# Performance work log

Measured on AMD Instinct MI355X. Metric: run time of the kernel, lower is better.

Reference implementation:

```python
import math
import jax, jax.numpy as jnp
import numpy as np

C, NH, NL, NP, NLAYERS, FFN = 256, 8, 3, 4, 6, 1024
DH = C // NH
SHAPES = ((64, 64), (32, 32), (16, 16))  # (H,W) for res3, res4, res5
SIZES = [h * w for h, w in SHAPES]
STARTS = np.cumsum([0] + SIZES[:-1]).tolist()
EPS = 1e-5


def _sin_pe(H, W):
    d = C // 4
    y = jnp.arange(H, dtype=jnp.float32)[:, None]
    x = jnp.arange(W, dtype=jnp.float32)[None, :]
    div = jnp.exp(jnp.arange(d, dtype=jnp.float32) * (-math.log(10000.0) / d))[:, None, None]
    pe = jnp.concatenate([
        jnp.broadcast_to(jnp.sin(y * div), (d, H, W)),
        jnp.broadcast_to(jnp.cos(y * div), (d, H, W)),
        jnp.broadcast_to(jnp.sin(x * div), (d, H, W)),
        jnp.broadcast_to(jnp.cos(x * div), (d, H, W)),
    ], axis=0)  # (C,H,W)
    return pe.reshape(C, H * W).T  # (HW, C)


def _ref_points():
    pts = []
    for H, W in SHAPES:
        y = jnp.linspace(0.5 / H, 1.0 - 0.5 / H, H)
        x = jnp.linspace(0.5 / W, 1.0 - 0.5 / W, W)
        ry, rx = jnp.meshgrid(y, x, indexing='ij')
        pts.append(jnp.stack([rx.ravel(), ry.ravel()], -1))
    return jnp.concatenate(pts, 0)[None, :, None, :]  # (1,N,1,2), same per level


def _layernorm(x, g, b):
    mu = x.mean(-1, keepdims=True)
    v = ((x - mu) ** 2).mean(-1, keepdims=True)
    return (x - mu) * jax.lax.rsqrt(v + EPS) * g + b


def _bilinear(v, loc, H, W):
    # v: (B,HW,NH,DH); loc: (B,N,NH,NP,2) in [0,1]; grid_sample align_corners=False, zero pad
    B, N = loc.shape[0], loc.shape[1]
    x = loc[..., 0] * W - 0.5
    y = loc[..., 1] * H - 0.5
    x0 = jnp.floor(x); y0 = jnp.floor(y)
    wx = x - x0; wy = y - y0
    x0i = x0.astype(jnp.int32); y0i = y0.astype(jnp.int32)
    v_t = jnp.transpose(v, (0, 2, 1, 3))  # (B,NH,HW,DH)

    def corner(xi, yi, w):
        valid = (xi >= 0) & (xi < W) & (yi >= 0) & (yi < H)
        idx = jnp.clip(yi, 0, H - 1) * W + jnp.clip(xi, 0, W - 1)  # (B,N,NH,NP)
        idx = jnp.transpose(idx, (0, 2, 1, 3)).reshape(B, NH, N * NP)
        g = jnp.take_along_axis(v_t, idx[..., None], axis=2)  # (B,NH,N*NP,DH)
        g = g.reshape(B, NH, N, NP, DH).transpose(0, 2, 1, 3, 4)
        return g * (w * valid)[..., None]

    return (corner(x0i, y0i, (1 - wx) * (1 - wy))
            + corner(x0i + 1, y0i, wx * (1 - wy))
            + corner(x0i, y0i + 1, (1 - wx) * wy)
            + corner(x0i + 1, y0i + 1, wx * wy))


def _forward(res2, res3, res4, res5, level_embed, off_W, off_b, aw_W, aw_b, val_W, val_b,
             out_W, out_b, ln1_g, ln1_b, fc1_W, fc1_b, fc2_W, fc2_b, ln2_g, ln2_b,
             lat_W, lat_b, sm_W, sm_b, gn_g, gn_b):
    feats = [res3, res4, res5]
    B = res3.shape[0]
    flat = jnp.concatenate(
        [f.reshape(B, C, -1).transpose(0, 2, 1) + level_embed[i] for i, f in enumerate(feats)], 1)
    pe = jnp.concatenate([_sin_pe(H, W) for H, W in SHAPES], 0)[None]  # (1,N,C)
    ref = _ref_points()  # (1,N,1,2)
    normalizer = jnp.array([[W, H] for H, W in SHAPES], jnp.float32)  # (NL,2) as (W,H)
    N = flat.shape[1]

    x = flat
    for l in range(NLAYERS):
        q = x + pe
        value = (x @ val_W[l].T + val_b[l]).reshape(B, N, NH, DH)
        off = (q @ off_W[l].T + off_b[l]).reshape(B, N, NH, NL, NP, 2)
        aw = jax.nn.softmax((q @ aw_W[l].T + aw_b[l]).reshape(B, N, NH, NL * NP), -1)
        aw = aw.reshape(B, N, NH, NL, NP)
        loc = ref[:, :, None, :, None, :] + off / normalizer[None, None, None, :, None, :]
        attn = jnp.zeros((B, N, NH, DH), x.dtype)
        for li, (H, W) in enumerate(SHAPES):
            v_l = value[:, STARTS[li]:STARTS[li] + SIZES[li]]
            samp = _bilinear(v_l, loc[:, :, :, li], H, W)  # (B,N,NH,NP,DH)
            attn = attn + jnp.einsum('bnhpd,bnhp->bnhd', samp, aw[:, :, :, li])
        attn = attn.reshape(B, N, C) @ out_W[l].T + out_b[l]
        x = _layernorm(x + attn, ln1_g[l], ln1_b[l])
        h = jax.nn.relu(x @ fc1_W[l].T + fc1_b[l]) @ fc2_W[l].T + fc2_b[l]
        x = _layernorm(x + h, ln2_g[l], ln2_b[l])

    outs = []
    for li, (H, W) in enumerate(SHAPES):
        tok = x[:, STARTS[li]:STARTS[li] + SIZES[li]]
        outs.append(tok.transpose(0, 2, 1).reshape(B, C, H, W))
    o3, o4, o5 = outs

    r2_lat = jnp.einsum('bchw,oc->bohw', res2, lat_W) + lat_b[None, :, None, None]
    Hr, Wr = res2.shape[2], res2.shape[3]
    r3_up = jax.image.resize(o3, (B, C, Hr, Wr), method='bilinear')
    s = jax.lax.conv_general_dilated(r2_lat + r3_up, sm_W, (1, 1), ((1, 1), (1, 1)),
                                     dimension_numbers=('NCHW', 'OIHW', 'NCHW'))
    s = s + sm_b[None, :, None, None]
    # GroupNorm(32, C)
    g = s.reshape(B, 32, C // 32, Hr, Wr)
    mu = g.mean((2, 3, 4), keepdims=True)
    var = jnp.var(g, axis=(2, 3, 4), keepdims=True)
    g = (g - mu) * jax.lax.rsqrt(var + EPS)
    s = g.reshape(B, C, Hr, Wr) * gn_g[None, :, None, None] + gn_b[None, :, None, None]
    s = jax.nn.gelu(s, approximate=False)
    return s, o3, o4, o5


def setup_inputs() -> dict:
    key = jax.random.key(0)
    ks = jax.random.split(key, 16)
    def rn(k, shape, s=0.02):
        return jax.random.normal(k, shape, jnp.float32) * s
    B = 2
    L = NLAYERS
    return {
        'res2': jax.random.normal(ks[0], (B, C, 128, 128), jnp.float32),
        'res3': jax.random.normal(ks[1], (B, C, 64, 64), jnp.float32),
        'res4': jax.random.normal(ks[2], (B, C, 32, 32), jnp.float32),
        'res5': jax.random.normal(ks[3], (B, C, 16, 16), jnp.float32),
        'level_embed': rn(ks[4], (NL, C)),
        'off_W': rn(ks[5], (L, NH * NL * NP * 2, C)), 'off_b': jnp.zeros((L, NH * NL * NP * 2)),
        'aw_W': rn(ks[6], (L, NH * NL * NP, C)), 'aw_b': jnp.zeros((L, NH * NL * NP)),
        'val_W': rn(ks[7], (L, C, C)), 'val_b': jnp.zeros((L, C)),
        'out_W': rn(ks[8], (L, C, C)), 'out_b': jnp.zeros((L, C)),
        'ln1_g': jnp.ones((L, C)), 'ln1_b': jnp.zeros((L, C)),
        'fc1_W': rn(ks[9], (L, FFN, C)), 'fc1_b': jnp.zeros((L, FFN)),
        'fc2_W': rn(ks[10], (L, C, FFN)), 'fc2_b': jnp.zeros((L, C)),
        'ln2_g': jnp.ones((L, C)), 'ln2_b': jnp.zeros((L, C)),
        'lat_W': rn(ks[11], (C, C)), 'lat_b': jnp.zeros((C,)),
        'sm_W': rn(ks[12], (C, C, 3, 3)), 'sm_b': jnp.zeros((C,)),
        'gn_g': jnp.ones((C,)), 'gn_b': jnp.zeros((C,)),
    }


def reference(res2, res3, res4, res5, level_embed, off_W, off_b, aw_W, aw_b, val_W, val_b,
              out_W, out_b, ln1_g, ln1_b, fc1_W, fc1_b, fc2_W, fc2_b, ln2_g, ln2_b,
              lat_W, lat_b, sm_W, sm_b, gn_g, gn_b):
    return _forward(res2, res3, res4, res5, level_embed, off_W, off_b, aw_W, aw_b,
                    val_W, val_b, out_W, out_b, ln1_g, ln1_b, fc1_W, fc1_b, fc2_W, fc2_b,
                    ln2_g, ln2_b, lat_W, lat_b, sm_W, sm_b, gn_g, gn_b)
```

## Files before the change

### kernel.cpp

```cpp
#include <hip/hip_runtime.h>

namespace {
constexpr int Bn   = 2;
constexpr int Cc   = 256;
constexpr int Ntok = 5376;
constexpr int Ffn  = 1024;
constexpr int HW2  = 128 * 128;
constexpr float EPSf = 1e-5f;
constexpr int WL   = 729088;
}

typedef __attribute__((ext_vector_type(8))) short bf16x8;
typedef __attribute__((ext_vector_type(4))) float f32x4;

__device__ inline unsigned short f2bf(float x) {
  unsigned u = __float_as_uint(x);
  return (unsigned short)((u + 0x7fffu + ((u >> 16) & 1u)) >> 16);
}
__device__ inline float bf2f(unsigned short b) {
  return __uint_as_float((unsigned)b << 16);
}

__device__ inline void store_chunk_f32(unsigned short* lds, int row, int g,
                                       const float* v8) {
  int sg = g ^ (row & 7);
  unsigned short tmp[8];
#pragma unroll
  for (int j = 0; j < 8; j++) tmp[j] = f2bf(v8[j]);
  *reinterpret_cast<uint4*>(&lds[row * 64 + sg * 8]) =
      *reinterpret_cast<const uint4*>(tmp);
}
__device__ inline void store_chunk_bf(unsigned short* lds, int row, int g,
                                      uint4 v) {
  int sg = g ^ (row & 7);
  *reinterpret_cast<uint4*>(&lds[row * 64 + sg * 8]) = v;
}

__global__ __launch_bounds__(256) void setup_all(
    const float* __restrict__ r3, const float* __restrict__ r4,
    const float* __restrict__ r5, const float* __restrict__ lemb,
    float* __restrict__ x, unsigned short* __restrict__ xb,
    unsigned short* __restrict__ qb, unsigned short* __restrict__ peb,
    const float* __restrict__ valW, const float* __restrict__ offW,
    const float* __restrict__ awW, const float* __restrict__ outW,
    const float* __restrict__ fc1W, const float* __restrict__ fc2W,
    const float* __restrict__ latW, const float* __restrict__ smW,
    unsigned short* __restrict__ wbf, unsigned short* __restrict__ wlat,
    unsigned short* __restrict__ wt) {
  int bx = blockIdx.x;
  int tid = threadIdx.x;
  if (bx < 1024) {
    const int NPC = Ntok * Cc;
    for (int i = bx * 256 + tid; i < Bn * NPC; i += 1024 * 256) {
      int c = i & 255;
      int rest = i >> 8;
      int p = rest % Ntok;
      int b = rest / Ntok;
      int li = (p < 4096) ? 0 : ((p < 5120) ? 1 : 2);
      int start = (li == 0) ? 0 : ((li == 1) ? 4096 : 5120);
      int size = (li == 0) ? 4096 : ((li == 1) ? 1024 : 256);
      const float* f = (li == 0) ? r3 : ((li == 1) ? r4 : r5);
      int sp = p - start;
      int shift = 6 - li;
      int W = 64 >> li;
      int iy = sp >> shift;
      int ix = sp & (W - 1);
      int j = c & 63;
      int sel = c >> 6;
      float div = expf(-(float)j * (9.210340371976184f / 64.f));
      float coord = (sel < 2) ? (float)iy : (float)ix;
      float arg = coord * div;
      unsigned short pe16 = f2bf((sel & 1) ? cosf(arg) : sinf(arg));
      float v = f[((size_t)(b * Cc + c)) * size + sp] + lemb[li * Cc + c];
      x[i] = v;
      xb[i] = f2bf(v);
      qb[i] = f2bf(v + bf2f(pe16));
      peb[i - b * NPC] = pe16;
    }
    return;
  }
  int b2 = bx - 1024;
  if (b2 < 4272) {
    int i4 = b2 * 256 + tid;
    int l = i4 / 182272;
    int e = (i4 - l * 182272) * 4;
    const float* src;
    int off;
    if (e < 65536) { src = valW + (size_t)l * 65536; off = e; }
    else if (e < 139264) {
      int j = e - 65536;
      if (j < 49152) { src = offW + (size_t)l * 49152; off = j; }
      else { src = awW + (size_t)l * 24576; off = j - 49152; }
    } else if (e < 204800) { src = outW + (size_t)l * 65536; off = e - 139264; }
    else if (e < 466944) { src = fc1W + (size_t)l * 262144; off = e - 204800; }
    else { src = fc2W + (size_t)l * 262144; off = e - 466944; }
    float4 v = *reinterpret_cast<const float4*>(&src[off]);
    unsigned short t[4] = {f2bf(v.x), f2bf(v.y), f2bf(v.z), f2bf(v.w)};
    *reinterpret_cast<uint2*>(&wbf[(size_t)l * WL + e]) =
        *reinterpret_cast<const uint2*>(t);
  } else if (b2 < 4336) {
    int e = ((b2 - 4272) * 256 + tid) * 4;
    float4 v = *reinterpret_cast<const float4*>(&latW[e]);
    unsigned short t[4] = {f2bf(v.x), f2bf(v.y), f2bf(v.z), f2bf(v.w)};
    *reinterpret_cast<uint2*>(&wlat[e]) = *reinterpret_cast<const uint2*>(t);
  } else {
    int i = (b2 - 4336) * 256 + tid;
    int o = i / 2304;
    int r = i - o * 2304;
    int tap = r >> 8;
    int c = r & 255;
    wt[i] = f2bf(smW[((size_t)(o * 256 + c)) * 9 + tap]);
  }
}

template <int ACT, int OBF>
__global__ __launch_bounds__(256) void gemm_mfma_b(
    const unsigned short* __restrict__ A, const unsigned short* __restrict__ Wb,
    const float* __restrict__ bias, void* __restrict__ outp,
    int M, int N, int K, int nbx) {
  __shared__ unsigned short As[64 * 64];
  __shared__ unsigned short Ws[128 * 64];
  const int tid = threadIdx.x;
  const int nwg = gridDim.x;
  const int swz = (blockIdx.x & 7) * (nwg >> 3) + (blockIdx.x >> 3);
  const int m0 = (swz / nbx) * 64, n0 = (swz % nbx) * 128;
  const int wid = tid >> 6, lane = tid & 63;
  const int wm = wid >> 1, wn = wid & 1;
  const int lr = lane & 15, lh = lane >> 4;
  const int r8 = tid >> 3, g8 = tid & 7;
  f32x4 acc[2][4];
#pragma unroll
  for (int i = 0; i < 2; i++)
#pragma unroll
    for (int j = 0; j < 4; j++) acc[i][j] = f32x4{0.f, 0.f, 0.f, 0.f};

  uint4 ra[2], rw[4];
  const uint4 z4 = uint4{0, 0, 0, 0};
#pragma unroll
  for (int i = 0; i < 2; i++)
    ra[i] = *reinterpret_cast<const uint4*>(
        &A[(size_t)(m0 + r8 + i * 32) * K + g8 * 8]);
#pragma unroll
  for (int i = 0; i < 4; i++) {
    int n = n0 + r8 + i * 32;
    rw[i] = (n < N) ? *reinterpret_cast<const uint4*>(
                          &Wb[(size_t)n * K + g8 * 8])
                    : z4;
  }

  for (int k0 = 0; k0 < K; k0 += 64) {
    if (k0) __syncthreads();
#pragma unroll
    for (int i = 0; i < 2; i++) store_chunk_bf(As, r8 + i * 32, g8, ra[i]);
#pragma unroll
    for (int i = 0; i < 4; i++) store_chunk_bf(Ws, r8 + i * 32, g8, rw[i]);
    __syncthreads();
    int kn = k0 + 64;
    if (kn < K) {
#pragma unroll
      for (int i = 0; i < 2; i++)
        ra[i] = *reinterpret_cast<const uint4*>(
            &A[(size_t)(m0 + r8 + i * 32) * K + kn + g8 * 8]);
#pragma unroll
      for (int i = 0; i < 4; i++) {
        int n = n0 + r8 + i * 32;
        rw[i] = (n < N) ? *reinterpret_cast<const uint4*>(
                              &Wb[(size_t)n * K + kn + g8 * 8])
                        : z4;
      }
    }
    bf16x8 af[2][2], bfr[4][2];
#pragma unroll
    for (int mi = 0; mi < 2; mi++) {
      int r = wm * 32 + mi * 16 + lr;
#pragma unroll
      for (int s = 0; s < 2; s++) {
        int g = s * 4 + lh;
        af[mi][s] =
            *reinterpret_cast<const bf16x8*>(&As[r * 64 + (g ^ (r & 7)) * 8]);
      }
    }
#pragma unroll
    for (int nj = 0; nj < 4; nj++) {
      int r = wn * 64 + nj * 16 + lr;
#pragma unroll
      for (int s = 0; s < 2; s++) {
        int g = s * 4 + lh;
        bfr[nj][s] =
            *reinterpret_cast<const bf16x8*>(&Ws[r * 64 + (g ^ (r & 7)) * 8]);
      }
    }
#pragma unroll
    for (int mi = 0; mi < 2; mi++)
#pragma unroll
      for (int nj = 0; nj < 4; nj++) {
        acc[mi][nj] = __builtin_amdgcn_mfma_f32_16x16x32_bf16(
            af[mi][0], bfr[nj][0], acc[mi][nj], 0, 0, 0);
        acc[mi][nj] = __builtin_amdgcn_mfma_f32_16x16x32_bf16(
            af[mi][1], bfr[nj][1], acc[mi][nj], 0, 0, 0);
      }
  }
#pragma unroll
  for (int mi = 0; mi < 2; mi++) {
    int row = m0 + wm * 32 + mi * 16 + lh * 4;
#pragma unroll
    for (int nj = 0; nj < 4; nj++) {
      int col = n0 + wn * 64 + nj * 16 + lr;
      if (col >= N) continue;
      float b = bias[col];
#pragma unroll
      for (int r = 0; r < 4; r++) {
        float v = acc[mi][nj][r] + b;
        if (ACT) v = fmaxf(v, 0.f);
        if (OBF)
          ((unsigned short*)outp)[(size_t)(row + r) * N + col] = f2bf(v);
        else
          ((float*)outp)[(size_t)(row + r) * N + col] = v;
      }
    }
  }
}

template <int WRITEQ, int TOKOUT>
__global__ __launch_bounds__(256) void gemm_ln(
    const unsigned short* __restrict__ A, const unsigned short* __restrict__ Wb,
    const float* __restrict__ bias, const float* __restrict__ g,
    const float* __restrict__ bta, float* __restrict__ x,
    unsigned short* __restrict__ xb, const unsigned short* __restrict__ peb,
    unsigned short* __restrict__ qb, int K, float* __restrict__ o3,
    float* __restrict__ o4, float* __restrict__ o5) {
  __shared__ unsigned short As[16 * 64];
  __shared__ unsigned short Ws[256 * 64];
  __shared__ float pred[4][16];
  __shared__ float qred[4][16];
  const int tid = threadIdx.x;
  const int swz = (blockIdx.x & 7) * 84 + (blockIdx.x >> 3);
  const int m0 = swz * 16;
  const int wid = tid >> 6, lane = tid & 63;
  const int lr = lane & 15, lh = lane >> 4;
  const int r8 = tid >> 3, g8 = tid & 7;
  f32x4 acc[4];
#pragma unroll
  for (int i = 0; i < 4; i++) acc[i] = f32x4{0.f, 0.f, 0.f, 0.f};

  uint4 ra, rw[8];
  if (tid < 128)
    ra = *reinterpret_cast<const uint4*>(&A[(size_t)(m0 + r8) * K + g8 * 8]);
#pragma unroll
  for (int i = 0; i < 8; i++)
    rw[i] = *reinterpret_cast<const uint4*>(
        &Wb[(size_t)(r8 + i * 32) * K + g8 * 8]);

  for (int k0 = 0; k0 < K; k0 += 64) {
    if (k0) __syncthreads();
    if (tid < 128) store_chunk_bf(As, r8, g8, ra);
#pragma unroll
    for (int i = 0; i < 8; i++) store_chunk_bf(Ws, r8 + i * 32, g8, rw[i]);
    __syncthreads();
    int kn = k0 + 64;
    if (kn < K) {
      if (tid < 128)
        ra = *reinterpret_cast<const uint4*>(
            &A[(size_t)(m0 + r8) * K + kn + g8 * 8]);
#pragma unroll
      for (int i = 0; i < 8; i++)
        rw[i] = *reinterpret_cast<const uint4*>(
            &Wb[(size_t)(r8 + i * 32) * K + kn + g8 * 8]);
    }
    bf16x8 af[2];
    {
      int r = lr;
#pragma unroll
      for (int s = 0; s < 2; s++) {
        int gg2 = s * 4 + lh;
        af[s] =
            *reinterpret_cast<const bf16x8*>(&As[r * 64 + (gg2 ^ (r & 7)) * 8]);
      }
    }
#pragma unroll
    for (int nt = 0; nt < 4; nt++) {
      int r = wid * 64 + nt * 16 + lr;
      bf16x8 b0 =
          *reinterpret_cast<const bf16x8*>(&Ws[r * 64 + (lh ^ (r & 7)) * 8]);
      bf16x8 b1 = *reinterpret_cast<const bf16x8*>(
          &Ws[r * 64 + ((4 + lh) ^ (r & 7)) * 8]);
      acc[nt] =
          __builtin_amdgcn_mfma_f32_16x16x32_bf16(af[0], b0, acc[nt], 0, 0, 0);
      acc[nt] =
          __builtin_amdgcn_mfma_f32_16x16x32_bf16(af[1], b1, acc[nt], 0, 0, 0);
    }
  }

  const int rowl = lh * 4;
#pragma unroll
  for (int nt = 0; nt < 4; nt++) {
    int col = wid * 64 + nt * 16 + lr;
    float bs = bias[col];
#pragma unroll
    for (int r = 0; r < 4; r++)
      acc[nt][r] += bs + x[(size_t)(m0 + rowl + r) * 256 + col];
  }
  float sum[4];
#pragma unroll
  for (int r = 0; r < 4; r++) {
    float s = 0.f;
#pragma unroll
    for (int nt = 0; nt < 4; nt++) s += acc[nt][r];
#pragma unroll
    for (int o = 8; o > 0; o >>= 1) s += __shfl_xor(s, o);
    sum[r] = s;
  }
  if (lr == 0) {
#pragma unroll
    for (int r = 0; r < 4; r++) pred[wid][lh * 4 + r] = sum[r];
  }
  __syncthreads();
  float mu[4];
#pragma unroll
  for (int r = 0; r < 4; r++)
    mu[r] = (pred[0][lh * 4 + r] + pred[1][lh * 4 + r] + pred[2][lh * 4 + r] +
             pred[3][lh * 4 + r]) *
            (1.f / 256.f);
  float qs[4];
#pragma unroll
  for (int r = 0; r < 4; r++) {
    float q = 0.f;
#pragma unroll
    for (int nt = 0; nt < 4; nt++) {
      float d = acc[nt][r] - mu[r];
      q += d * d;
    }
#pragma unroll
    for (int o = 8; o > 0; o >>= 1) q += __shfl_xor(q, o);
    qs[r] = q;
  }
  if (lr == 0) {
#pragma unroll
    for (int r = 0; r < 4; r++) qred[wid][lh * 4 + r] = qs[r];
  }
  __syncthreads();
  float rstd[4];
#pragma unroll
  for (int r = 0; r < 4; r++)
    rstd[r] = rsqrtf((qred[0][lh * 4 + r] + qred[1][lh * 4 + r] +
                      qred[2][lh * 4 + r] + qred[3][lh * 4 + r]) *
                         (1.f / 256.f) +
                     EPSf);
  float oarr[4][4];
#pragma unroll
  for (int nt = 0; nt < 4; nt++) {
    int col = wid * 64 + nt * 16 + lr;
    float gw = g[col], bw = bta[col];
#pragma unroll
    for (int r = 0; r < 4; r++) {
      int row = m0 + rowl + r;
      size_t idx = (size_t)row * 256 + col;
      float o = (acc[nt][r] - mu[r]) * rstd[r] * gw + bw;
      x[idx] = o;
      xb[idx] = f2bf(o);
      if (WRITEQ) {
        size_t pc = idx - (row >= Ntok ? (size_t)Ntok * 256 : 0);
        qb[idx] = f2bf(o + bf2f(peb[pc]));
      }
      if (TOKOUT) oarr[nt][r] = o;
    }
  }
  if constexpr (TOKOUT) {
    __shared__ float tout[16][129];
    int bb = (m0 >= Ntok) ? 1 : 0;
    int n = m0 - bb * Ntok;
    float* outp;
    int osize, ostart;
    if (n < 4096) { outp = o3; osize = 4096; ostart = 0; }
    else if (n < 5120) { outp = o4; osize = 1024; ostart = 4096; }
    else { outp = o5; osize = 256; ostart = 5120; }
    int sp0 = n - ostart;
#pragma unroll
    for (int hh = 0; hh < 2; hh++) {
      __syncthreads();
      if ((wid >> 1) == hh) {
#pragma unroll
        for (int nt = 0; nt < 4; nt++) {
          int cl = (wid & 1) * 64 + nt * 16 + lr;
#pragma unroll
          for (int r = 0; r < 4; r++) tout[rowl + r][cl] = oarr[nt][r];
        }
      }
      __syncthreads();
      int cl = tid & 127, rh = tid >> 7;
      float* dst =
          outp + ((size_t)(bb * 256 + hh * 128 + cl)) * osize + sp0 + rh * 8;
#pragma unroll
      for (int i = 0; i < 8; i += 4) {
        float4 v4 = {tout[rh * 8 + i + 0][cl], tout[rh * 8 + i + 1][cl],
                     tout[rh * 8 + i + 2][cl], tout[rh * 8 + i + 3][cl]};
        *reinterpret_cast<float4*>(&dst[i]) = v4;
      }
    }
  }
}

__global__ __launch_bounds__(256) void gemm_head(
    const unsigned short* __restrict__ xb, const unsigned short* __restrict__ qb,
    const unsigned short* __restrict__ wv, const unsigned short* __restrict__ wo,
    const float* __restrict__ valB, const float* __restrict__ offB,
    const float* __restrict__ awB, unsigned short* __restrict__ valO,
    float* __restrict__ offO, float* __restrict__ awO) {
  __shared__ unsigned short As[32 * 64];
  __shared__ unsigned short Ws[128 * 64];
  const int tid = threadIdx.x;
  const int swz = (blockIdx.x & 7) * 210 + (blockIdx.x >> 3);
  const bool isval = swz < 672;
  const unsigned short* A;
  const unsigned short* W;
  int m0, n0, Nn;
  if (isval) {
    A = xb; W = wv; Nn = 256;
    m0 = (swz >> 1) * 32; n0 = (swz & 1) * 128;
  } else {
    int s = swz - 672;
    A = qb; W = wo; Nn = 288;
    m0 = (s / 3) * 32; n0 = (s % 3) * 128;
  }
  const int wid = tid >> 6, lane = tid & 63;
  const int wm = wid >> 1, wn = wid & 1;
  const int lr = lane & 15, lh = lane >> 4;
  const int r8 = tid >> 3, g8 = tid & 7;
  f32x4 acc[4];
#pragma unroll
  for (int j = 0; j < 4; j++) acc[j] = f32x4{0.f, 0.f, 0.f, 0.f};

  uint4 ra, rw[4];
  const uint4 z4 = uint4{0, 0, 0, 0};
  ra = *reinterpret_cast<const uint4*>(&A[(size_t)(m0 + r8) * 256 + g8 * 8]);
#pragma unroll
  for (int i = 0; i < 4; i++) {
    int n = n0 + r8 + i * 32;
    rw[i] = (n < Nn) ? *reinterpret_cast<const uint4*>(
                           &W[(size_t)n * 256 + g8 * 8])
                     : z4;
  }

  for (int k0 = 0; k0 < 256; k0 += 64) {
    if (k0) __syncthreads();
    store_chunk_bf(As, r8, g8, ra);
#pragma unroll
    for (int i = 0; i < 4; i++) store_chunk_bf(Ws, r8 + i * 32, g8, rw[i]);
    __syncthreads();
    int kn = k0 + 64;
    if (kn < 256) {
      ra = *reinterpret_cast<const uint4*>(
          &A[(size_t)(m0 + r8) * 256 + kn + g8 * 8]);
#pragma unroll
      for (int i = 0; i < 4; i++) {
        int n = n0 + r8 + i * 32;
        rw[i] = (n < Nn) ? *reinterpret_cast<const uint4*>(
                               &W[(size_t)n * 256 + kn + g8 * 8])
                         : z4;
      }
    }
    bf16x8 af[2];
    {
      int r = wm * 16 + lr;
#pragma unroll
      for (int s = 0; s < 2; s++) {
        int gg2 = s * 4 + lh;
        af[s] =
            *reinterpret_cast<const bf16x8*>(&As[r * 64 + (gg2 ^ (r & 7)) * 8]);
      }
    }
#pragma unroll
    for (int nj = 0; nj < 4; nj++) {
      int r = wn * 64 + nj * 16 + lr;
      bf16x8 b0 =
          *reinterpret_cast<const bf16x8*>(&Ws[r * 64 + (lh ^ (r & 7)) * 8]);
      bf16x8 b1 = *reinterpret_cast<const bf16x8*>(
          &Ws[r * 64 + ((4 + lh) ^ (r & 7)) * 8]);
      acc[nj] =
          __builtin_amdgcn_mfma_f32_16x16x32_bf16(af[0], b0, acc[nj], 0, 0, 0);
      acc[nj] =
          __builtin_amdgcn_mfma_f32_16x16x32_bf16(af[1], b1, acc[nj], 0, 0, 0);
    }
  }
  const int row0 = m0 + wm * 16 + lh * 4;
#pragma unroll
  for (int nj = 0; nj < 4; nj++) {
    int col = n0 + wn * 64 + nj * 16 + lr;
    if (isval) {
      float b = valB[col];
#pragma unroll
      for (int r = 0; r < 4; r++)
        valO[(size_t)(row0 + r) * 256 + col] = f2bf(acc[nj][r] + b);
    } else {
      if (col >= 288) continue;
      float b = (col < 192) ? offB[col] : awB[col - 192];
#pragma unroll
      for (int r = 0; r < 4; r++) {
        float v = acc[nj][r] + b;
        if (col < 192)
          offO[(size_t)(row0 + r) * 192 + col] = v;
        else
          awO[(size_t)(row0 + r) * 96 + col - 192] = v;
      }
    }
  }
}

__global__ __launch_bounds__(256) void msda_fused(
    const unsigned short* __restrict__ value, const float* __restrict__ off,
    const float* __restrict__ awl, unsigned short* __restrict__ attn) {
  __shared__ int recI[16][12][4];
  __shared__ float recW[16][12][4];
  __shared__ float els[16][12];
  const int tid = threadIdx.x;
  float e = 0.f;
  int idxr[4];
  float wcr[4];
  int gq = 0, p = 0;
  if (tid < 192) {
    gq = tid / 12;
    p = tid - gq * 12;
    int gid = blockIdx.x * 16 + gq;
    int h = gid & 7;
    int bn = gid >> 3;
    int n = bn % Ntok;
    int b = bn / Ntok;
    int li0 = (n < 4096) ? 0 : ((n < 5120) ? 1 : 2);
    int start0 = (li0 == 0) ? 0 : ((li0 == 1) ? 4096 : 5120);
    int shift = 6 - li0;
    int Wn = 1 << shift;
    int sp = n - start0;
    int iy = sp >> shift;
    int ix = sp & (Wn - 1);
    float refx = (ix + 0.5f) / (float)Wn;
    float refy = (iy + 0.5f) / (float)Wn;
    const float* ap = awl + (size_t)bn * 96 + h * 12;
    float lg[12];
    float mx = -1e30f;
#pragma unroll
    for (int j = 0; j < 12; j++) { lg[j] = ap[j]; mx = fmaxf(mx, lg[j]); }
    e = expf(lg[p] - mx);
    els[gq][p] = e;
    int li = p >> 2;
    int HWl = 64 >> li;
    int st = (li == 0) ? 0 : ((li == 1) ? 4096 : 5120);
    const float* op = off + (size_t)bn * 192 + h * 24;
    float ox = op[p * 2 + 0];
    float oy = op[p * 2 + 1];
    float lx = refx + ox / (float)HWl;
    float ly = refy + oy / (float)HWl;
    float fx = lx * (float)HWl - 0.5f;
    float fy = ly * (float)HWl - 0.5f;
    float x0f = floorf(fx), y0f = floorf(fy);
    float wx = fx - x0f, wy = fy - y0f;
    int ix0 = (int)x0f, iy0 = (int)y0f;
    int base = (b * Ntok + st) * 256 + h * 32;
#pragma unroll
    for (int cr = 0; cr < 4; cr++) {
      int cx = ix0 + (cr & 1);
      int cy = iy0 + (cr >> 1);
      bool valid = (cx >= 0) & (cx < HWl) & (cy >= 0) & (cy < HWl);
      float wc = ((cr & 1) ? wx : 1.f - wx) * ((cr >> 1) ? wy : 1.f - wy);
      int cxc = min(max(cx, 0), HWl - 1);
      int cyc = min(max(cy, 0), HWl - 1);
      idxr[cr] = base + (cyc * HWl + cxc) * 256;
      wcr[cr] = valid ? wc : 0.f;
    }
  }
  __syncthreads();
  if (tid < 192) {
    float ssum = 0.f;
#pragma unroll
    for (int j = 0; j < 12; j++) ssum += els[gq][j];
    float w = e / ssum;
#pragma unroll
    for (int cr = 0; cr < 4; cr++) {
      recI[gq][p][cr] = idxr[cr];
      recW[gq][p][cr] = w * wcr[cr];
    }
  }
  __syncthreads();
  const int grp = tid >> 4, lane = tid & 15;
  const unsigned short* vb = value + lane * 2;
  float acc0 = 0.f, acc1 = 0.f;
#pragma unroll
  for (int pp = 0; pp < 12; pp++) {
    int4 idx = *reinterpret_cast<const int4*>(&recI[grp][pp][0]);
    float4 w = *reinterpret_cast<const float4*>(&recW[grp][pp][0]);
    unsigned ua = *reinterpret_cast<const unsigned*>(&vb[idx.x]);
    unsigned ub = *reinterpret_cast<const unsigned*>(&vb[idx.y]);
    unsigned uc = *reinterpret_cast<const unsigned*>(&vb[idx.z]);
    unsigned ud = *reinterpret_cast<const unsigned*>(&vb[idx.w]);
    acc0 += w.x * bf2f((unsigned short)(ua & 0xffff));
    acc1 += w.x * bf2f((unsigned short)(ua >> 16));
    acc0 += w.y * bf2f((unsigned short)(ub & 0xffff));
    acc1 += w.y * bf2f((unsigned short)(ub >> 16));
    acc0 += w.z * bf2f((unsigned short)(uc & 0xffff));
    acc1 += w.z * bf2f((unsigned short)(uc >> 16));
    acc0 += w.w * bf2f((unsigned short)(ud & 0xffff));
    acc1 += w.w * bf2f((unsigned short)(ud >> 16));
  }
  int gid = blockIdx.x * 16 + grp;
  unsigned outw = (unsigned)f2bf(acc0) | ((unsigned)f2bf(acc1) << 16);
  *reinterpret_cast<unsigned*>(&attn[(size_t)gid * 32 + lane * 2]) = outw;
}

__global__ __launch_bounds__(256) void conv3x3_mfma(
    const unsigned short* __restrict__ T, const unsigned short* __restrict__ Wt,
    const float* __restrict__ bias, unsigned short* __restrict__ out) {
  __shared__ unsigned short As[64 * 64];
  __shared__ unsigned short Ws[128 * 64];
  const int tid = threadIdx.x;
  const int nwg = gridDim.x;
  const int swz = (blockIdx.x & 7) * (nwg >> 3) + (blockIdx.x >> 3);
  const int m0 = (swz >> 1) * 64, n0 = (swz & 1) * 128;
  const int b = m0 >> 14;
  const int p0 = m0 & 16383;
  const int y = p0 >> 7;
  const int x0 = p0 & 127;
  const int wid = tid >> 6, lane = tid & 63;
  const int wm = wid >> 1, wn = wid & 1;
  const int lr = lane & 15, lh = lane >> 4;
  const int r8 = tid >> 3, g8 = tid & 7;
  f32x4 acc[2][4];
#pragma unroll
  for (int i = 0; i < 2; i++)
#pragma unroll
    for (int j = 0; j < 4; j++) acc[i][j] = f32x4{0.f, 0.f, 0.f, 0.f};

  uint4 ra[2], rw[4];
  auto loadA = [&](int kc, uint4* r) {
    int tap = kc >> 2;
    int cb = (kc & 3) * 64;
    int dy = tap / 3 - 1, dx = tap % 3 - 1;
    int yy = y + dy;
#pragma unroll
    for (int i = 0; i < 2; i++) {
      int row = r8 + i * 32;
      int xx = x0 + row + dx;
      uint4 v = uint4{0, 0, 0, 0};
      if (yy >= 0 && yy < 128 && xx >= 0 && xx < 128)
        v = *reinterpret_cast<const uint4*>(
            &T[((size_t)(b * 16384 + yy * 128 + xx)) * 256 + cb + g8 * 8]);
      r[i] = v;
    }
  };
  auto loadW = [&](int kc, uint4* r) {
#pragma unroll
    for (int i = 0; i < 4; i++)
      r[i] = *reinterpret_cast<const uint4*>(
          &Wt[(size_t)(n0 + r8 + i * 32) * 2304 + kc * 64 + g8 * 8]);
  };
  loadA(0, ra);
  loadW(0, rw);

  for (int kc = 0; kc < 36; kc++) {
    if (kc) __syncthreads();
#pragma unroll
    for (int i = 0; i < 2; i++) store_chunk_bf(As, r8 + i * 32, g8, ra[i]);
#pragma unroll
    for (int i = 0; i < 4; i++) store_chunk_bf(Ws, r8 + i * 32, g8, rw[i]);
    __syncthreads();
    if (kc + 1 < 36) {
      loadA(kc + 1, ra);
      loadW(kc + 1, rw);
    }
    bf16x8 af[2][2], bfr[4][2];
#pragma unroll
    for (int mi = 0; mi < 2; mi++) {
      int r = wm * 32 + mi * 16 + lr;
#pragma unroll
      for (int s = 0; s < 2; s++) {
        int g = s * 4 + lh;
        af[mi][s] =
            *reinterpret_cast<const bf16x8*>(&As[r * 64 + (g ^ (r & 7)) * 8]);
      }
    }
#pragma unroll
    for (int nj = 0; nj < 4; nj++) {
      int r = wn * 64 + nj * 16 + lr;
#pragma unroll
      for (int s = 0; s < 2; s++) {
        int g = s * 4 + lh;
        bfr[nj][s] =
            *reinterpret_cast<const bf16x8*>(&Ws[r * 64 + (g ^ (r & 7)) * 8]);
      }
    }
#pragma unroll
    for (int mi = 0; mi < 2; mi++)
#pragma unroll
      for (int nj = 0; nj < 4; nj++) {
        acc[mi][nj] = __builtin_amdgcn_mfma_f32_16x16x32_bf16(
            af[mi][0], bfr[nj][0], acc[mi][nj], 0, 0, 0);
        acc[mi][nj] = __builtin_amdgcn_mfma_f32_16x16x32_bf16(
            af[mi][1], bfr[nj][1], acc[mi][nj], 0, 0, 0);
      }
  }
#pragma unroll
  for (int mi = 0; mi < 2; mi++) {
    int row = m0 + wm * 32 + mi * 16 + lh * 4;
#pragma unroll
    for (int nj = 0; nj < 4; nj++) {
      int col = n0 + wn * 64 + nj * 16 + lr;
      float b = bias[col];
#pragma unroll
      for (int r = 0; r < 4; r++)
        out[(size_t)(row + r) * 256 + col] = f2bf(acc[mi][nj][r] + b);
    }
  }
}

__global__ __launch_bounds__(256) void gemm_tn_mfma(
    const float* __restrict__ A, const unsigned short* __restrict__ Wb,
    const float* __restrict__ bias, const float* __restrict__ x,
    unsigned short* __restrict__ out) {
  __shared__ unsigned short As[64 * 64];
  __shared__ unsigned short Ws[128 * 64];
  const int tid = threadIdx.x;
  const int nwg = gridDim.x;
  const int swz = (blockIdx.x & 7) * (nwg >> 3) + (blockIdx.x >> 3);
  const int m0 = (swz >> 1) * 64, n0 = (swz & 1) * 128;
  const int b = m0 >> 14;
  const int p0 = m0 & 16383;
  const int wid = tid >> 6, lane = tid & 63;
  const int wm = wid >> 1, wn = wid & 1;
  const int lr = lane & 15, lh = lane >> 4;
  const int r8 = tid >> 3, g8 = tid & 7;
  const int arow = tid & 63, agb = tid >> 6;
  f32x4 acc[2][4];
#pragma unroll
  for (int i = 0; i < 2; i++)
#pragma unroll
    for (int j = 0; j < 4; j++) acc[i][j] = f32x4{0.f, 0.f, 0.f, 0.f};

  float va[16];
  uint4 rw[4];
  auto loadA = [&](int k0, float* v) {
#pragma unroll
    for (int i = 0; i < 2; i++) {
      int g = agb + i * 4;
#pragma unroll
      for (int j = 0; j < 8; j++)
        v[i * 8 + j] =
            A[(size_t)(b * 256 + k0 + g * 8 + j) * 16384 + p0 + arow];
    }
  };
  auto loadW = [&](int k0, uint4* r) {
#pragma unroll
    for (int i = 0; i < 4; i++)
      r[i] = *reinterpret_cast<const uint4*>(
          &Wb[(size_t)(n0 + r8 + i * 32) * 256 + k0 + g8 * 8]);
  };
  loadA(0, va);
  loadW(0, rw);

  for (int k0 = 0; k0 < 256; k0 += 64) {
    if (k0) __syncthreads();
#pragma unroll
    for (int i = 0; i < 2; i++)
      store_chunk_f32(As, arow, agb + i * 4, &va[i * 8]);
#pragma unroll
    for (int i = 0; i < 4; i++) store_chunk_bf(Ws, r8 + i * 32, g8, rw[i]);
    __syncthreads();
    int kn = k0 + 64;
    if (kn < 256) {
      loadA(kn, va);
      loadW(kn, rw);
    }
    bf16x8 af[2][2], bfr[4][2];
#pragma unroll
    for (int mi = 0; mi < 2; mi++) {
      int r = wm * 32 + mi * 16 + lr;
#pragma unroll
      for (int s = 0; s < 2; s++) {
        int g = s * 4 + lh;
        af[mi][s] =
            *reinterpret_cast<const bf16x8*>(&As[r * 64 + (g ^ (r & 7)) * 8]);
      }
    }
#pragma unroll
    for (int nj = 0; nj < 4; nj++) {
      int r = wn * 64 + nj * 16 + lr;
#pragma unroll
      for (int s = 0; s < 2; s++) {
        int g = s * 4 + lh;
        bfr[nj][s] =
            *reinterpret_cast<const bf16x8*>(&Ws[r * 64 + (g ^ (r & 7)) * 8]);
      }
    }
#pragma unroll
    for (int mi = 0; mi < 2; mi++)
#pragma unroll
      for (int nj = 0; nj < 4; nj++) {
        acc[mi][nj] = __builtin_amdgcn_mfma_f32_16x16x32_bf16(
            af[mi][0], bfr[nj][0], acc[mi][nj], 0, 0, 0);
        acc[mi][nj] = __builtin_amdgcn_mfma_f32_16x16x32_bf16(
            af[mi][1], bfr[nj][1], acc[mi][nj], 0, 0, 0);
      }
  }
  const float* xbse = x + (size_t)b * Ntok * 256;
#pragma unroll
  for (int mi = 0; mi < 2; mi++) {
    int row0 = m0 + wm * 32 + mi * 16 + lh * 4;
#pragma unroll
    for (int r = 0; r < 4; r++) {
      int p = (row0 + r) & 16383;
      int Y = p >> 7, X = p & 127;
      float yc = Y * 0.5f - 0.25f;
      float y0f = floorf(yc);
      float wy = yc - y0f;
      int y0 = (int)y0f;
      int y0c = min(max(y0, 0), 63), y1c = min(max(y0 + 1, 0), 63);
      float xc = X * 0.5f - 0.25f;
      float x0f = floorf(xc);
      float wx = xc - x0f;
      int xq0 = (int)x0f;
      int x0c = min(max(xq0, 0), 63), x1c = min(max(xq0 + 1, 0), 63);
      const float* r00 = xbse + (size_t)(y0c * 64 + x0c) * 256;
      const float* r01 = xbse + (size_t)(y0c * 64 + x1c) * 256;
      const float* r10 = xbse + (size_t)(y1c * 64 + x0c) * 256;
      const float* r11 = xbse + (size_t)(y1c * 64 + x1c) * 256;
#pragma unroll
      for (int nj = 0; nj < 4; nj++) {
        int col = n0 + wn * 64 + nj * 16 + lr;
        float up = (1.f - wy) * ((1.f - wx) * r00[col] + wx * r01[col]) +
                   wy * ((1.f - wx) * r10[col] + wx * r11[col]);
        out[(size_t)(row0 + r) * 256 + col] =
            f2bf(acc[mi][nj][r] + bias[col] + up);
      }
    }
  }
}

__global__ __launch_bounds__(256) void gn_partial(
    const unsigned short* __restrict__ s, float* __restrict__ part) {
  int blk = blockIdx.x;
  int pr = blk & 15;
  int bg = blk >> 4;
  int g = bg & 31;
  int b = bg >> 5;
  int tid = threadIdx.x;
  float sum = 0.f, sq = 0.f;
  for (int e = pr * 8192 + tid; e < (pr + 1) * 8192; e += 256) {
    int p = e >> 3, cc = e & 7;
    float v = bf2f(s[((size_t)(b * 16384 + p)) * 256 + g * 8 + cc]);
    sum += v;
    sq += v * v;
  }
  __shared__ float rs[256], rq[256];
  rs[tid] = sum;
  rq[tid] = sq;
  __syncthreads();
  for (int st = 128; st > 0; st >>= 1) {
    if (tid < st) { rs[tid] += rs[tid + st]; rq[tid] += rq[tid + st]; }
    __syncthreads();
  }
  if (tid == 0) {
    part[(size_t)blk * 2 + 0] = rs[0];
    part[(size_t)blk * 2 + 1] = rq[0];
  }
}

__global__ void gn_final(const float* __restrict__ part,
                         float* __restrict__ stats) {
  int tid = threadIdx.x;
  if (tid < 64) {
    float s = 0.f, q = 0.f;
    for (int j = 0; j < 16; j++) {
      s += part[(size_t)(tid * 16 + j) * 2 + 0];
      q += part[(size_t)(tid * 16 + j) * 2 + 1];
    }
    float mu = s * (1.f / 131072.f);
    float var = q * (1.f / 131072.f) - mu * mu;
    stats[tid * 2 + 0] = mu;
    stats[tid * 2 + 1] = rsqrtf(var + EPSf);
  }
}

__global__ void gn_apply(const unsigned short* __restrict__ s,
                         const float* __restrict__ stats,
                         const float* __restrict__ gg,
                         const float* __restrict__ gb,
                         float* __restrict__ out) {
  __shared__ float tile[32][33];
  int p0 = blockIdx.x * 32, c0 = blockIdx.y * 32, b = blockIdx.z;
  int tx = threadIdx.x, tyy = threadIdx.y;
  int c = c0 + tx;
  float mu = stats[(b * 32 + (c >> 3)) * 2 + 0];
  float rstd = stats[(b * 32 + (c >> 3)) * 2 + 1];
  float gw = gg[c], bw = gb[c];
  for (int i = tyy; i < 32; i += 8) {
    float v = bf2f(s[((size_t)(b * 16384 + p0 + i)) * 256 + c]);
    v = (v - mu) * rstd * gw + bw;
    v = 0.5f * v * (1.f + erff(v * 0.70710678118654752f));
    tile[i][tx] = v;
  }
  __syncthreads();
  for (int i = tyy; i < 32; i += 8)
    out[((size_t)(b * 256 + c0 + i)) * 16384 + p0 + tx] = tile[tx][i];
}

extern "C" void kernel_launch(void* const* d_in, const int* in_sizes, int n_in,
                              void* d_out, int out_size, void* d_ws,
                              size_t ws_size, hipStream_t stream) {
  (void)in_sizes; (void)n_in; (void)out_size; (void)ws_size;
  const float* res2  = (const float*)d_in[0];
  const float* res3  = (const float*)d_in[1];
  const float* res4  = (const float*)d_in[2];
  const float* res5  = (const float*)d_in[3];
  const float* lemb  = (const float*)d_in[4];
  const float* off_W = (const float*)d_in[5];
  const float* off_b = (const float*)d_in[6];
  const float* aw_W  = (const float*)d_in[7];
  const float* aw_b  = (const float*)d_in[8];
  const float* val_W = (const float*)d_in[9];
  const float* val_b = (const float*)d_in[10];
  const float* out_W = (const float*)d_in[11];
  const float* out_b = (const float*)d_in[12];
  const float* ln1_g = (const float*)d_in[13];
  const float* ln1_b = (const float*)d_in[14];
  const float* fc1_W = (const float*)d_in[15];
  const float* fc1_b = (const float*)d_in[16];
  const float* fc2_W = (const float*)d_in[17];
  const float* fc2_b = (const float*)d_in[18];
  const float* ln2_g = (const float*)d_in[19];
  const float* ln2_b = (const float*)d_in[20];
  const float* lat_W = (const float*)d_in[21];
  const float* lat_b = (const float*)d_in[22];
  const float* sm_W  = (const float*)d_in[23];
  const float* sm_b  = (const float*)d_in[24];
  const float* gn_g  = (const float*)d_in[25];
  const float* gn_b  = (const float*)d_in[26];

  float* ws = (float*)d_ws;
  float*          x      = ws;
  unsigned short* xb     = (unsigned short*)(ws + 2752512);
  unsigned short* peb    = (unsigned short*)(ws + 4128768);
  unsigned short* qb     = (unsigned short*)(ws + 4816896);
  unsigned short* valueb = (unsigned short*)(ws + 6193152);
  float*          offb   = ws + 7569408;
  float*          awl    = ws + 9633792;
  unsigned short* attnb  = (unsigned short*)(ws + 10665984);
  unsigned short* hb     = (unsigned short*)(ws + 14794752);
  unsigned short* tbuf   = hb;
  unsigned short* wtbuf  = (unsigned short*)(ws + 20299776);
  float*          gnpart = ws + 20594688;
  float*          gnstat = ws + 20596736;
  unsigned short* wbf    = (unsigned short*)(ws + 20596864);
  unsigned short* wlat   = wbf + (size_t)6 * WL;
  unsigned short* sbufb  = (unsigned short*)ws;

  float* out_s  = (float*)d_out;
  float* out_o3 = out_s + (size_t)Bn * Cc * HW2;
  float* out_o4 = out_o3 + (size_t)Bn * Cc * 4096;
  float* out_o5 = out_o4 + (size_t)Bn * Cc * 1024;

  const int M = Bn * Ntok;

  setup_all<<<7664, 256, 0, stream>>>(res3, res4, res5, lemb, x, xb, qb, peb,
                                      val_W, off_W, aw_W, out_W, fc1_W, fc2_W,
                                      lat_W, sm_W, wbf, wlat, wtbuf);

  for (int l = 0; l < 6; l++) {
    const unsigned short* wl = wbf + (size_t)l * WL;
    gemm_head<<<1680, 256, 0, stream>>>(
        xb, qb, wl + 0, wl + 65536, val_b + l * 256, off_b + l * 192,
        aw_b + l * 96, valueb, offb, awl);
    msda_fused<<<5376, 256, 0, stream>>>(valueb, offb, awl, attnb);
    gemm_ln<0, 0><<<672, 256, 0, stream>>>(
        attnb, wl + 139264, out_b + l * 256, ln1_g + l * 256, ln1_b + l * 256,
        x, xb, peb, qb, 256, nullptr, nullptr, nullptr);
    gemm_mfma_b<1, 1><<<1344, 256, 0, stream>>>(
        xb, wl + 204800, fc1_b + l * 1024, hb, M, 1024, 256, 8);
    if (l < 5)
      gemm_ln<1, 0><<<672, 256, 0, stream>>>(
          hb, wl + 466944, fc2_b + l * 256, ln2_g + l * 256, ln2_b + l * 256,
          x, xb, peb, qb, 1024, nullptr, nullptr, nullptr);
    else
      gemm_ln<0, 1><<<672, 256, 0, stream>>>(
          hb, wl + 466944, fc2_b + l * 256, ln2_g + l * 256, ln2_b + l * 256,
          x, xb, peb, qb, 1024, out_o3, out_o4, out_o5);
  }

  gemm_tn_mfma<<<1024, 256, 0, stream>>>(res2, wlat, lat_b, x, tbuf);
  conv3x3_mfma<<<1024, 256, 0, stream>>>(tbuf, wtbuf, sm_b, sbufb);
  gn_partial<<<1024, 256, 0, stream>>>(sbufb, gnpart);
  gn_final<<<1, 64, 0, stream>>>(gnpart, gnstat);
  gn_apply<<<dim3(512, 8, 2), dim3(32, 8), 0, stream>>>(sbufb, gnstat, gn_g,
                                                        gn_b, out_s);
}
```

Measured before the change: 671.7 us.

## Fuse deformable-attention sampling into output projection with residual LayerNorm

Replaces the separate sampling kernel and the out-projection GEMM+LN kernel with one kernel. Each block first computes softmaxed bilinear sampling records for 16 tokens and stages them in LDS. It then gathers the value vectors into an LDS bf16 tile and runs the MFMA out-projection, bias, residual add and LayerNorm in the same block. This removes one launch per layer and the global write and re-read of the attention output. In exchange, the gather runs on far fewer threads (672 blocks instead of 5376), which can reduce latency hiding, and the sampling weights are now rounded to bf16.

Measured after the change: 639.8 us. 4.8% less time.

```diff
diff --git a/kernel.cpp b/kernel.cpp
--- a/kernel.cpp
+++ b/kernel.cpp
@@ -400,6 +400,244 @@
   }
 }
 
+__global__ __launch_bounds__(256) void msda_out_ln(
+    const unsigned short* __restrict__ value, const float* __restrict__ off,
+    const float* __restrict__ awl, const unsigned short* __restrict__ Wb,
+    const float* __restrict__ bias, const float* __restrict__ g,
+    const float* __restrict__ bta, float* __restrict__ x,
+    unsigned short* __restrict__ xb) {
+  __shared__ unsigned short Ws[256 * 64];
+  __shared__ unsigned short atile[4][16 * 64];
+  __shared__ float pred[4][16];
+  __shared__ float qred[4][16];
+  const int tid = threadIdx.x;
+  const int swz = (blockIdx.x & 7) * 84 + (blockIdx.x >> 3);
+  const int m0 = swz * 16;
+  const int wid = tid >> 6, lane = tid & 63;
+  const int lr = lane & 15, lh = lane >> 4;
+  const int r8 = tid >> 3, g8 = tid & 7;
+
+  uint4 rw[8];
+#pragma unroll
+  for (int i = 0; i < 8; i++)
+    rw[i] = *reinterpret_cast<const uint4*>(
+        &Wb[(size_t)(r8 + i * 32) * 256 + g8 * 8]);
+
+  unsigned short* rec = Ws;
+  if (tid < 128) {
+    int row = m0 + (tid >> 3);
+    int h = tid & 7;
+    int n = row % Ntok;
+    int li0 = (n < 4096) ? 0 : ((n < 5120) ? 1 : 2);
+    int start0 = (li0 == 0) ? 0 : ((li0 == 1) ? 4096 : 5120);
+    int shift = 6 - li0;
+    int Wn = 1 << shift;
+    int sp = n - start0;
+    int iy = sp >> shift;
+    int ix = sp & (Wn - 1);
+    float refx = (ix + 0.5f) / (float)Wn;
+    float refy = (iy + 0.5f) / (float)Wn;
+    const float* ap = awl + (size_t)row * 96 + h * 12;
+    float lg[12];
+    float mx = -1e30f;
+#pragma unroll
+    for (int j = 0; j < 12; j++) { lg[j] = ap[j]; mx = fmaxf(mx, lg[j]); }
+    float ssum = 0.f;
+#pragma unroll
+    for (int j = 0; j < 12; j++) { lg[j] = expf(lg[j] - mx); ssum += lg[j]; }
+    const float* op = off + (size_t)row * 192 + h * 24;
+#pragma unroll
+    for (int p = 0; p < 12; p++) {
+      int li = p >> 2;
+      int HWl = 64 >> li;
+      float w = lg[p] / ssum;
+      float ox = op[p * 2 + 0];
+      float oy = op[p * 2 + 1];
+      float lx = refx + ox / (float)HWl;
+      float ly = refy + oy / (float)HWl;
+      float fx = lx * (float)HWl - 0.5f;
+      float fy = ly * (float)HWl - 0.5f;
+      float x0f = floorf(fx), y0f = floorf(fy);
+      float wx = fx - x0f, wy = fy - y0f;
+      int ix0 = (int)x0f, iy0 = (int)y0f;
+      unsigned short sp4[4], w4[4];
+#pragma unroll
+      for (int cr = 0; cr < 4; cr++) {
+        int cx = ix0 + (cr & 1);
+        int cy = iy0 + (cr >> 1);
+        bool valid = (cx >= 0) & (cx < HWl) & (cy >= 0) & (cy < HWl);
+        float wc = ((cr & 1) ? wx : 1.f - wx) * ((cr >> 1) ? wy : 1.f - wy);
+        int cxc = min(max(cx, 0), HWl - 1);
+        int cyc = min(max(cy, 0), HWl - 1);
+        sp4[cr] = (unsigned short)(cyc * HWl + cxc);
+        w4[cr] = f2bf(valid ? (w * wc) : 0.f);
+      }
+      *reinterpret_cast<uint2*>(&rec[(tid * 12 + p) * 8]) =
+          *reinterpret_cast<const uint2*>(sp4);
+      *reinterpret_cast<uint2*>(&rec[(tid * 12 + p) * 8 + 4]) =
+          *reinterpret_cast<const uint2*>(w4);
+    }
+  }
+  __syncthreads();
+  {
+    int gq = tid >> 1;
+    int half = tid & 1;
+    int rr = gq >> 3;
+    int row = m0 + rr;
+    int h = gq & 7;
+    int b = (row >= Ntok) ? 1 : 0;
+    int coff = h * 32 + half * 16;
+    int base0 = (b * Ntok + 0) * 256 + coff;
+    int base1 = (b * Ntok + 4096) * 256 + coff;
+    int base2 = (b * Ntok + 5120) * 256 + coff;
+    float acc[16];
+#pragma unroll
+    for (int j = 0; j < 16; j++) acc[j] = 0.f;
+    const unsigned short* rp = rec + gq * 96;
+#pragma unroll
+    for (int p = 0; p < 12; p++) {
+      int li = p >> 2;
+      int base = (li == 0) ? base0 : ((li == 1) ? base1 : base2);
+      unsigned short sp4[4], w4[4];
+      *reinterpret_cast<uint2*>(sp4) =
+          *reinterpret_cast<const uint2*>(&rp[p * 8]);
+      *reinterpret_cast<uint2*>(w4) =
+          *reinterpret_cast<const uint2*>(&rp[p * 8 + 4]);
+#pragma unroll
+      for (int cr = 0; cr < 4; cr++) {
+        float w = bf2f(w4[cr]);
+        const unsigned short* vsrc = value + base + (int)sp4[cr] * 256;
+#pragma unroll
+        for (int j = 0; j < 8; j++) {
+          unsigned u = *reinterpret_cast<const unsigned*>(&vsrc[j * 2]);
+          acc[j * 2 + 0] += w * bf2f((unsigned short)(u & 0xffff));
+          acc[j * 2 + 1] += w * bf2f((unsigned short)(u >> 16));
+        }
+      }
+    }
+#pragma unroll
+    for (int j = 0; j < 8; j++) {
+      int c0 = coff + j * 2;
+      int kc = c0 >> 6;
+      int cc = c0 & 63;
+      int ggr = cc >> 3, el = cc & 7;
+      unsigned outw =
+          (unsigned)f2bf(acc[j * 2]) | ((unsigned)f2bf(acc[j * 2 + 1]) << 16);
+      *reinterpret_cast<unsigned*>(
+          &atile[kc][rr * 64 + ((ggr ^ (rr & 7)) * 8) + el]) = outw;
+    }
+  }
+  __syncthreads();
+
+  f32x4 acc[4];
+#pragma unroll
+  for (int i = 0; i < 4; i++) acc[i] = f32x4{0.f, 0.f, 0.f, 0.f};
+  for (int k0 = 0; k0 < 256; k0 += 64) {
+    if (k0) __syncthreads();
+#pragma unroll
+    for (int i = 0; i < 8; i++) store_chunk_bf(Ws, r8 + i * 32, g8, rw[i]);
+    __syncthreads();
+    int kn = k0 + 64;
+    if (kn < 256) {
+#pragma unroll
+      for (int i = 0; i < 8; i++)
+        rw[i] = *reinterpret_cast<const uint4*>(
+            &Wb[(size_t)(r8 + i * 32) * 256 + kn + g8 * 8]);
+    }
+    bf16x8 af[2];
+    {
+      int r = lr;
+#pragma unroll
+      for (int s = 0; s < 2; s++) {
+        int gg2 = s * 4 + lh;
+        af[s] = *reinterpret_cast<const bf16x8*>(
+            &atile[k0 >> 6][r * 64 + (gg2 ^ (r & 7)) * 8]);
+      }
+    }
+#pragma unroll
+    for (int nt = 0; nt < 4; nt++) {
+      int r = wid * 64 + nt * 16 + lr;
+      bf16x8 b0 =
+          *reinterpret_cast<const bf16x8*>(&Ws[r * 64 + (lh ^ (r & 7)) * 8]);
+      bf16x8 b1 = *reinterpret_cast<const bf16x8*>(
+          &Ws[r * 64 + ((4 + lh) ^ (r & 7)) * 8]);
+      acc[nt] =
+          __builtin_amdgcn_mfma_f32_16x16x32_bf16(af[0], b0, acc[nt], 0, 0, 0);
+      acc[nt] =
+          __builtin_amdgcn_mfma_f32_16x16x32_bf16(af[1], b1, acc[nt], 0, 0, 0);
+    }
+  }
+
+  const int rowl = lh * 4;
+#pragma unroll
+  for (int nt = 0; nt < 4; nt++) {
+    int col = wid * 64 + nt * 16 + lr;
+    float bs = bias[col];
+#pragma unroll
+    for (int r = 0; r < 4; r++)
+      acc[nt][r] += bs + x[(size_t)(m0 + rowl + r) * 256 + col];
+  }
+  float sum[4];
+#pragma unroll
+  for (int r = 0; r < 4; r++) {
+    float s = 0.f;
+#pragma unroll
+    for (int nt = 0; nt < 4; nt++) s += acc[nt][r];
+#pragma unroll
+    for (int o = 8; o > 0; o >>= 1) s += __shfl_xor(s, o);
+    sum[r] = s;
+  }
+  if (lr == 0) {
+#pragma unroll
+    for (int r = 0; r < 4; r++) pred[wid][lh * 4 + r] = sum[r];
+  }
+  __syncthreads();
+  float mu[4];
+#pragma unroll
+  for (int r = 0; r < 4; r++)
+    mu[r] = (pred[0][lh * 4 + r] + pred[1][lh * 4 + r] + pred[2][lh * 4 + r] +
+             pred[3][lh * 4 + r]) *
+            (1.f / 256.f);
+  float qs[4];
+#pragma unroll
+  for (int r = 0; r < 4; r++) {
+    float q = 0.f;
+#pragma unroll
+    for (int nt = 0; nt < 4; nt++) {
+      float d = acc[nt][r] - mu[r];
+      q += d * d;
+    }
+#pragma unroll
+    for (int o = 8; o > 0; o >>= 1) q += __shfl_xor(q, o);
+    qs[r] = q;
+  }
+  if (lr == 0) {
+#pragma unroll
+    for (int r = 0; r < 4; r++) qred[wid][lh * 4 + r] = qs[r];
+  }
+  __syncthreads();
+  float rstd[4];
+#pragma unroll
+  for (int r = 0; r < 4; r++)
+    rstd[r] = rsqrtf((qred[0][lh * 4 + r] + qred[1][lh * 4 + r] +
+                      qred[2][lh * 4 + r] + qred[3][lh * 4 + r]) *
+                         (1.f / 256.f) +
+                     EPSf);
+#pragma unroll
+  for (int nt = 0; nt < 4; nt++) {
+    int col = wid * 64 + nt * 16 + lr;
+    float gw = g[col], bw = bta[col];
+#pragma unroll
+    for (int r = 0; r < 4; r++) {
+      int row = m0 + rowl + r;
+      size_t idx = (size_t)row * 256 + col;
+      float o = (acc[nt][r] - mu[r]) * rstd[r] * gw + bw;
+      x[idx] = o;
+      xb[idx] = f2bf(o);
+    }
+  }
+}
+
 __global__ __launch_bounds__(256) void gemm_head(
     const unsigned short* __restrict__ xb, const unsigned short* __restrict__ qb,
     const unsigned short* __restrict__ wv, const unsigned short* __restrict__ wo,
@@ -504,105 +742,6 @@
       }
     }
   }
-}
-
-__global__ __launch_bounds__(256) void msda_fused(
-    const unsigned short* __restrict__ value, const float* __restrict__ off,
-    const float* __restrict__ awl, unsigned short* __restrict__ attn) {
-  __shared__ int recI[16][12][4];
-  __shared__ float recW[16][12][4];
-  __shared__ float els[16][12];
-  const int tid = threadIdx.x;
-  float e = 0.f;
-  int idxr[4];
-  float wcr[4];
-  int gq = 0, p = 0;
-  if (tid < 192) {
-    gq = tid / 12;
-    p = tid - gq * 12;
-    int gid = blockIdx.x * 16 + gq;
-    int h = gid & 7;
-    int bn = gid >> 3;
-    int n = bn % Ntok;
-    int b = bn / Ntok;
-    int li0 = (n < 4096) ? 0 : ((n < 5120) ? 1 : 2);
-    int start0 = (li0 == 0) ? 0 : ((li0 == 1) ? 4096 : 5120);
-    int shift = 6 - li0;
-    int Wn = 1 << shift;
-    int sp = n - start0;
-    int iy = sp >> shift;
-    int ix = sp & (Wn - 1);
-    float refx = (ix + 0.5f) / (float)Wn;
-    float refy = (iy + 0.5f) / (float)Wn;
-    const float* ap = awl + (size_t)bn * 96 + h * 12;
-    float lg[12];
-    float mx = -1e30f;
-#pragma unroll
-    for (int j = 0; j < 12; j++) { lg[j] = ap[j]; mx = fmaxf(mx, lg[j]); }
-    e = expf(lg[p] - mx);
-    els[gq][p] = e;
-    int li = p >> 2;
-    int HWl = 64 >> li;
-    int st = (li == 0) ? 0 : ((li == 1) ? 4096 : 5120);
-    const float* op = off + (size_t)bn * 192 + h * 24;
-    float ox = op[p * 2 + 0];
-    float oy = op[p * 2 + 1];
-    float lx = refx + ox / (float)HWl;
-    float ly = refy + oy / (float)HWl;
-    float fx = lx * (float)HWl - 0.5f;
-    float fy = ly * (float)HWl - 0.5f;
-    float x0f = floorf(fx), y0f = floorf(fy);
-    float wx = fx - x0f, wy = fy - y0f;
-    int ix0 = (int)x0f, iy0 = (int)y0f;
-    int base = (b * Ntok + st) * 256 + h * 32;
-#pragma unroll
-    for (int cr = 0; cr < 4; cr++) {
-      int cx = ix0 + (cr & 1);
-      int cy = iy0 + (cr >> 1);
-      bool valid = (cx >= 0) & (cx < HWl) & (cy >= 0) & (cy < HWl);
-      float wc = ((cr & 1) ? wx : 1.f - wx) * ((cr >> 1) ? wy : 1.f - wy);
-      int cxc = min(max(cx, 0), HWl - 1);
-      int cyc = min(max(cy, 0), HWl - 1);
-      idxr[cr] = base + (cyc * HWl + cxc) * 256;
-      wcr[cr] = valid ? wc : 0.f;
-    }
-  }
-  __syncthreads();
-  if (tid < 192) {
-    float ssum = 0.f;
-#pragma unroll
-    for (int j = 0; j < 12; j++) ssum += els[gq][j];
-    float w = e / ssum;
-#pragma unroll
-    for (int cr = 0; cr < 4; cr++) {
-      recI[gq][p][cr] = idxr[cr];
-      recW[gq][p][cr] = w * wcr[cr];
-    }
-  }
-  __syncthreads();
-  const int grp = tid >> 4, lane = tid & 15;
-  const unsigned short* vb = value + lane * 2;
-  float acc0 = 0.f, acc1 = 0.f;
-#pragma unroll
-  for (int pp = 0; pp < 12; pp++) {
-    int4 idx = *reinterpret_cast<const int4*>(&recI[grp][pp][0]);
-    float4 w = *reinterpret_cast<const float4*>(&recW[grp][pp][0]);
-    unsigned ua = *reinterpret_cast<const unsigned*>(&vb[idx.x]);
-    unsigned ub = *reinterpret_cast<const unsigned*>(&vb[idx.y]);
-    unsigned uc = *reinterpret_cast<const unsigned*>(&vb[idx.z]);
-    unsigned ud = *reinterpret_cast<const unsigned*>(&vb[idx.w]);
-    acc0 += w.x * bf2f((unsigned short)(ua & 0xffff));
-    acc1 += w.x * bf2f((unsigned short)(ua >> 16));
-    acc0 += w.y * bf2f((unsigned short)(ub & 0xffff));
-    acc1 += w.y * bf2f((unsigned short)(ub >> 16));
-    acc0 += w.z * bf2f((unsigned short)(uc & 0xffff));
-    acc1 += w.z * bf2f((unsigned short)(uc >> 16));
-    acc0 += w.w * bf2f((unsigned short)(ud & 0xffff));
-    acc1 += w.w * bf2f((unsigned short)(ud >> 16));
-  }
-  int gid = blockIdx.x * 16 + grp;
-  unsigned outw = (unsigned)f2bf(acc0) | ((unsigned)f2bf(acc1) << 16);
-  *reinterpret_cast<unsigned*>(&attn[(size_t)gid * 32 + lane * 2]) = outw;
 }
 
 __global__ __launch_bounds__(256) void conv3x3_mfma(
@@ -940,7 +1079,6 @@
   unsigned short* valueb = (unsigned short*)(ws + 6193152);
   float*          offb   = ws + 7569408;
   float*          awl    = ws + 9633792;
-  unsigned short* attnb  = (unsigned short*)(ws + 10665984);
   unsigned short* hb     = (unsigned short*)(ws + 14794752);
   unsigned short* tbuf   = hb;
   unsigned short* wtbuf  = (unsigned short*)(ws + 20299776);
@@ -966,10 +1104,9 @@
     gemm_head<<<1680, 256, 0, stream>>>(
         xb, qb, wl + 0, wl + 65536, val_b + l * 256, off_b + l * 192,
         aw_b + l * 96, valueb, offb, awl);
-    msda_fused<<<5376, 256, 0, stream>>>(valueb, offb, awl, attnb);
-    gemm_ln<0, 0><<<672, 256, 0, stream>>>(
-        attnb, wl + 139264, out_b + l * 256, ln1_g + l * 256, ln1_b + l * 256,
-        x, xb, peb, qb, 256, nullptr, nullptr, nullptr);
+    msda_out_ln<<<672, 256, 0, stream>>>(
+        valueb, offb, awl, wl + 139264, out_b + l * 256, ln1_g + l * 256,
+        ln1_b + l * 256, x, xb);
     gemm_mfma_b<1, 1><<<1344, 256, 0, stream>>>(
         xb, wl + 204800, fc1_b + l * 1024, hb, M, 1024, 256, 8);
     if (l < 5)
```
